# Kernel optimization log

Hardware: AMD Instinct MI355X
Metric: run time of the kernel (lower is better)

The kernel has to match this reference:

```python
import jax, jax.numpy as jnp
import numpy as np
import math

D_MODEL, D_K, D_V = 1024, 64, 64
B, S = 4, 4096


def setup_inputs() -> dict:
    key = jax.random.key(0)
    ks = jax.random.split(key, 7)
    lim = 1.0 / math.sqrt(D_MODEL)
    return {
        "embeddings": jax.random.normal(ks[0], (B, S, D_MODEL), dtype=jnp.float32),
        "Wq": jax.random.uniform(ks[1], (D_MODEL, D_K), minval=-lim, maxval=lim, dtype=jnp.float32),
        "bq": jax.random.uniform(ks[2], (D_K,), minval=-lim, maxval=lim, dtype=jnp.float32),
        "Wk": jax.random.uniform(ks[3], (D_MODEL, D_K), minval=-lim, maxval=lim, dtype=jnp.float32),
        "bk": jax.random.uniform(ks[4], (D_K,), minval=-lim, maxval=lim, dtype=jnp.float32),
        "Wv": jax.random.uniform(ks[5], (D_MODEL, D_V), minval=-lim, maxval=lim, dtype=jnp.float32),
        "bv": jax.random.uniform(ks[6], (D_V,), minval=-lim, maxval=lim, dtype=jnp.float32),
    }


def reference(embeddings, Wq, bq, Wk, bk, Wv, bv):
    # Q, K: [B, S, d_k]; V: [B, S, d_v]
    Q = embeddings @ Wq + bq
    K = embeddings @ Wk + bk
    V = embeddings @ Wv + bv
    scale = 1.0 / math.sqrt(D_K)
    # scores: [B, S, S]
    scores = jnp.einsum("bsk,btk->bst", Q, K) * scale
    attn = jax.nn.softmax(scores, axis=-1)
    return jnp.einsum("bst,btv->bsv", attn, V)
```

## Files before the change

### kernel.cpp

```cpp
#include <hip/hip_runtime.h>

#define SEQ  4096
#define DMODEL 1024
#define QTOT 16384
#define QSCALE 0.18033688011112042f

typedef __bf16 bf16x8 __attribute__((ext_vector_type(8)));
typedef unsigned short u16x8 __attribute__((ext_vector_type(8)));
typedef float f32x4 __attribute__((ext_vector_type(4)));

static __device__ __forceinline__ unsigned short f2bfbits(float f) {
    unsigned int u = __builtin_bit_cast(unsigned int, f);
    unsigned int lsb = (u >> 16) & 1u;
    u += 0x7fffu + lsb;
    return (unsigned short)(u >> 16);
}

static __device__ __forceinline__ bf16x8 ld_frag(const unsigned short* p) {
    uint4 u = *reinterpret_cast<const uint4*>(p);
    return __builtin_bit_cast(bf16x8, u);
}

__global__ void prep_weights(const float* __restrict__ Wq,
                             const float* __restrict__ Wk,
                             const float* __restrict__ Wv,
                             unsigned short* __restrict__ WtS) {
    int o = blockIdx.x * 256 + threadIdx.x;
    int f = o >> 9, q = o & 511;
    int lane = q >> 3, j = q & 7;
    int kc = f / 12, nt = f - kc * 12;
    int n = nt * 16 + (lane & 15);
    int k = kc * 32 + (lane >> 4) * 8 + j;
    float v;
    if (n < 64)       v = Wq[k * 64 + n];
    else if (n < 128) v = Wk[k * 64 + (n - 64)];
    else              v = Wv[k * 64 + (n - 128)];
    WtS[o] = f2bfbits(v);
}

__global__ __launch_bounds__(256) void proj_cs(
        const float* __restrict__ emb, const unsigned short* __restrict__ WtS,
        const float* __restrict__ bq, const float* __restrict__ bk,
        const float* __restrict__ bv,
        unsigned short* __restrict__ Qb, unsigned short* __restrict__ Kb,
        unsigned short* __restrict__ VT) {
    __shared__ __align__(16) unsigned short Et[2][32 * 256];

    const int tid = threadIdx.x;
    const int w = tid >> 6, lane = tid & 63;
    const int c = lane & 15, qd = lane >> 4;
    const int m = w & 1, nh = w >> 1;
    const int mbase = blockIdx.x * 32;

    f32x4 acc[6];
#pragma unroll
    for (int i = 0; i < 6; i++) acc[i] = (f32x4){0.f, 0.f, 0.f, 0.f};

    const unsigned short* wpB = WtS + nh * 3072 + lane * 8;

    {
        float4 g[8];
#pragma unroll
        for (int rr = 0; rr < 8; rr++)
            g[rr] = *reinterpret_cast<const float4*>(
                emb + (size_t)(mbase + w * 8 + rr) * DMODEL + lane * 4);
#pragma unroll
        for (int rr = 0; rr < 8; rr++) {
            int row = w * 8 + rr;
            ushort4 p;
            p.x = f2bfbits(g[rr].x); p.y = f2bfbits(g[rr].y);
            p.z = f2bfbits(g[rr].z); p.w = f2bfbits(g[rr].w);
            int off = (lane * 8) ^ ((row & 7) << 4);
            *reinterpret_cast<ushort4*>(
                reinterpret_cast<char*>(&Et[0][0]) + row * 512 + off) = p;
        }
    }

    bf16x8 wc[6];
#pragma unroll
    for (int jj = 0; jj < 6; jj++) wc[jj] = ld_frag(wpB + jj * 512);

    __syncthreads();

    int cur = 0;
    for (int mega = 0; mega < 4; mega++) {
        float4 g[8];
        if (mega < 3) {
#pragma unroll
            for (int rr = 0; rr < 8; rr++)
                g[rr] = *reinterpret_cast<const float4*>(
                    emb + (size_t)(mbase + w * 8 + rr) * DMODEL
                        + (mega + 1) * 256 + lane * 4);
        }

        const char* Eb = reinterpret_cast<const char*>(&Et[cur][0]);
        bf16x8 aq[8];
#pragma unroll
        for (int ks = 0; ks < 8; ks++) {
            int off = (ks * 64 + qd * 16) ^ ((c & 7) << 4);
            aq[ks] = ld_frag(reinterpret_cast<const unsigned short*>(
                Eb + (m * 16 + c) * 512 + off));
        }

#pragma unroll
        for (int ks = 0; ks < 8; ks++) {
            int s = mega * 8 + ks;
            bf16x8 wn[6];
            if (s < 31) {
#pragma unroll
                for (int jj = 0; jj < 6; jj++)
                    wn[jj] = ld_frag(wpB + (s + 1) * 6144 + jj * 512);
            } else {
#pragma unroll
                for (int jj = 0; jj < 6; jj++) wn[jj] = wc[jj];
            }
#pragma unroll
            for (int jj = 0; jj < 6; jj++)
                acc[jj] = __builtin_amdgcn_mfma_f32_16x16x32_bf16(aq[ks], wc[jj], acc[jj], 0, 0, 0);
#pragma unroll
            for (int jj = 0; jj < 6; jj++) wc[jj] = wn[jj];
        }

        if (mega < 3) {
#pragma unroll
            for (int rr = 0; rr < 8; rr++) {
                int row = w * 8 + rr;
                ushort4 p;
                p.x = f2bfbits(g[rr].x); p.y = f2bfbits(g[rr].y);
                p.z = f2bfbits(g[rr].z); p.w = f2bfbits(g[rr].w);
                int off = (lane * 8) ^ ((row & 7) << 4);
                *reinterpret_cast<ushort4*>(
                    reinterpret_cast<char*>(&Et[cur ^ 1][0]) + row * 512 + off) = p;
            }
        }
        __syncthreads();
        cur ^= 1;
    }

#pragma unroll
    for (int jj = 0; jj < 6; jj++) {
        int n = (nh * 6 + jj) * 16 + c;
        float bias = (n < 64) ? bq[n] : (n < 128) ? bk[n - 64] : bv[n - 128];
        float fac = (n < 64) ? QSCALE : 1.0f;
#pragma unroll
        for (int r = 0; r < 4; r++) {
            int token = mbase + m * 16 + qd * 4 + r;
            unsigned short bits = f2bfbits((acc[jj][r] + bias) * fac);
            if (n < 64)        Qb[(size_t)token * 64 + n] = bits;
            else if (n < 128)  Kb[(size_t)token * 64 + (n - 64)] = bits;
            else {
                int bb = token >> 12, ss = token & 4095;
                VT[((size_t)bb * 64 + (n - 128)) * SEQ + ss] = bits;
            }
        }
    }
}

__global__ __launch_bounds__(512, 2) void attn(
        const unsigned short* __restrict__ Qb, const unsigned short* __restrict__ Kb,
        const unsigned short* __restrict__ VT, float* __restrict__ out) {
    __shared__ __align__(16) unsigned short Pl[8][64 * 72];
    __shared__ float l_all[8][64];

    const int tid = threadIdx.x;
    const int w = tid >> 6, lane = tid & 63;
    const int c = lane & 15, qd = lane >> 4;
    const int g3 = blockIdx.x & 7;
    const int b = g3 >> 1;
    const int qblk = ((blockIdx.x >> 3) << 1) | (g3 & 1);
    const int qbase = qblk * 64;
    const int tstart = w * 512;

    bf16x8 aq0[4], aq1[4];
#pragma unroll
    for (int qs = 0; qs < 4; qs++) {
        const unsigned short* Qp = Qb + ((size_t)(b << 12) + qbase + qs * 16 + c) * 64 + qd * 8;
        aq0[qs] = ld_frag(Qp);
        aq1[qs] = ld_frag(Qp + 32);
    }

    f32x4 acc[16];
#pragma unroll
    for (int i = 0; i < 16; i++) acc[i] = (f32x4){0.f, 0.f, 0.f, 0.f};
    float lsum[4][4];
#pragma unroll
    for (int qs = 0; qs < 4; qs++)
#pragma unroll
        for (int r = 0; r < 4; r++) lsum[qs][r] = 0.f;

    unsigned short* myP = &Pl[w][0];

#pragma unroll 2
    for (int it = 0; it < 8; it++) {
        const int t0 = tstart + it * 64;
        const unsigned short* Kt = Kb + ((size_t)(b << 12) + t0) * 64;

        bf16x8 bk0[4], bk1[4];
#pragma unroll
        for (int ts = 0; ts < 4; ts++) {
            bk0[ts] = ld_frag(Kt + (ts * 16 + c) * 64 + qd * 8);
            bk1[ts] = ld_frag(Kt + (ts * 16 + c) * 64 + 32 + qd * 8);
        }

#pragma unroll
        for (int qs = 0; qs < 4; qs++) {
            f32x4 sc[4];
#pragma unroll
            for (int ts = 0; ts < 4; ts++) {
                f32x4 z = (f32x4){0.f, 0.f, 0.f, 0.f};
                z = __builtin_amdgcn_mfma_f32_16x16x32_bf16(aq0[qs], bk0[ts], z, 0, 0, 0);
                z = __builtin_amdgcn_mfma_f32_16x16x32_bf16(aq1[qs], bk1[ts], z, 0, 0, 0);
                sc[ts] = z;
            }
#pragma unroll
            for (int ts = 0; ts < 4; ts++)
#pragma unroll
                for (int r = 0; r < 4; r++) {
                    float p = __builtin_amdgcn_exp2f(sc[ts][r]);
                    lsum[qs][r] += p;
                    myP[(qs * 16 + qd * 4 + r) * 72 + ts * 16 + c] = f2bfbits(p);
                }
        }

        bf16x8 bv0[4], bv1[4];
#pragma unroll
        for (int nt = 0; nt < 4; nt++) {
            const unsigned short* Vp = VT + (((size_t)b * 64 + nt * 16 + c) << 12) + t0 + qd * 8;
            bv0[nt] = ld_frag(Vp);
            bv1[nt] = ld_frag(Vp + 32);
        }

#pragma unroll
        for (int qs = 0; qs < 4; qs++) {
            bf16x8 ap0 = ld_frag(&myP[(qs * 16 + c) * 72 + qd * 8]);
            bf16x8 ap1 = ld_frag(&myP[(qs * 16 + c) * 72 + 32 + qd * 8]);
#pragma unroll
            for (int nt = 0; nt < 4; nt++) {
                acc[qs * 4 + nt] = __builtin_amdgcn_mfma_f32_16x16x32_bf16(ap0, bv0[nt], acc[qs * 4 + nt], 0, 0, 0);
                acc[qs * 4 + nt] = __builtin_amdgcn_mfma_f32_16x16x32_bf16(ap1, bv1[nt], acc[qs * 4 + nt], 0, 0, 0);
            }
        }
    }

#pragma unroll
    for (int off = 1; off < 16; off <<= 1)
#pragma unroll
        for (int qs = 0; qs < 4; qs++)
#pragma unroll
            for (int r = 0; r < 4; r++) lsum[qs][r] += __shfl_xor(lsum[qs][r], off);
    if (c == 0) {
#pragma unroll
        for (int qs = 0; qs < 4; qs++)
#pragma unroll
            for (int r = 0; r < 4; r++)
                l_all[w][qs * 16 + qd * 4 + r] = lsum[qs][r];
    }

    float* red = (float*)&Pl[0][0];
    __syncthreads();
    if (w >= 4) {
        float* rp = red + (w - 4) * 4352 + lane * 68;
#pragma unroll
        for (int i = 0; i < 16; i++) *reinterpret_cast<f32x4*>(rp + i * 4) = acc[i];
    }
    __syncthreads();
    if (w < 4) {
        float* rp = red + w * 4352 + lane * 68;
#pragma unroll
        for (int i = 0; i < 16; i++) acc[i] += *reinterpret_cast<const f32x4*>(rp + i * 4);
    }
    __syncthreads();
    if (w == 2 || w == 3) {
        float* rp = red + (w - 2) * 4352 + lane * 68;
#pragma unroll
        for (int i = 0; i < 16; i++) *reinterpret_cast<f32x4*>(rp + i * 4) = acc[i];
    }
    __syncthreads();
    if (w < 2) {
        float* rp = red + w * 4352 + lane * 68;
#pragma unroll
        for (int i = 0; i < 16; i++) acc[i] += *reinterpret_cast<const f32x4*>(rp + i * 4);
    }
    __syncthreads();
    if (w == 1) {
        float* rp = red + lane * 68;
#pragma unroll
        for (int i = 0; i < 16; i++) *reinterpret_cast<f32x4*>(rp + i * 4) = acc[i];
    }
    __syncthreads();
    if (w == 0) {
        float* rp = red + lane * 68;
#pragma unroll
        for (int i = 0; i < 16; i++) acc[i] += *reinterpret_cast<const f32x4*>(rp + i * 4);
#pragma unroll
        for (int qs = 0; qs < 4; qs++)
#pragma unroll
            for (int r = 0; r < 4; r++) {
                int q = qs * 16 + qd * 4 + r;
                float l = 0.f;
#pragma unroll
                for (int ww = 0; ww < 8; ww++) l += l_all[ww][q];
                float inv = 1.0f / l;
                size_t row = (size_t)(b << 12) + qbase + q;
#pragma unroll
                for (int nt = 0; nt < 4; nt++)
                    out[row * 64 + nt * 16 + c] = acc[qs * 4 + nt][r] * inv;
            }
    }
}

extern "C" void kernel_launch(void* const* d_in, const int* in_sizes, int n_in,
                              void* d_out, int out_size, void* d_ws, size_t ws_size,
                              hipStream_t stream) {
    const float* emb = (const float*)d_in[0];
    const float* Wq  = (const float*)d_in[1];
    const float* bq  = (const float*)d_in[2];
    const float* Wk  = (const float*)d_in[3];
    const float* bk  = (const float*)d_in[4];
    const float* Wv  = (const float*)d_in[5];
    const float* bv  = (const float*)d_in[6];
    float* out = (float*)d_out;

    unsigned short* ws = (unsigned short*)d_ws;
    unsigned short* WtS = ws;
    unsigned short* Qb = ws + 192 * 1024;
    unsigned short* Kb = Qb + QTOT * 64;
    unsigned short* VT = Kb + QTOT * 64;

    prep_weights<<<768, 256, 0, stream>>>(Wq, Wk, Wv, WtS);
    proj_cs<<<512, 256, 0, stream>>>(emb, WtS, bq, bk, bv, Qb, Kb, VT);
    attn<<<256, 512, 0, stream>>>(Qb, Kb, VT, out);
}
```

Baseline: 153.7 us.

## Split attention key range across two blocks and add finalize reduction kernel

The attention kernel now processes half the key range per block: grid doubles to 512 blocks, each wave covers 256 keys instead of 512. Unnormalized accumulators and row sums are written to workspace, and a new finalize kernel sums the two halves and normalizes. This is meant to raise occupancy across CUs (256 blocks underfilled the device), at the cost of extra global traffic for partials and one more kernel launch. It relies on softmax with no max subtraction, so the partials combine additively.

```diff
diff --git a/kernel.cpp b/kernel.cpp
--- a/kernel.cpp
+++ b/kernel.cpp
@@ -158,7 +158,8 @@
 
 __global__ __launch_bounds__(512, 2) void attn(
         const unsigned short* __restrict__ Qb, const unsigned short* __restrict__ Kb,
-        const unsigned short* __restrict__ VT, float* __restrict__ out) {
+        const unsigned short* __restrict__ VT,
+        float* __restrict__ accP, float* __restrict__ lsumP) {
     __shared__ __align__(16) unsigned short Pl[8][64 * 72];
     __shared__ float l_all[8][64];
 
@@ -167,9 +168,10 @@
     const int c = lane & 15, qd = lane >> 4;
     const int g3 = blockIdx.x & 7;
     const int b = g3 >> 1;
-    const int qblk = ((blockIdx.x >> 3) << 1) | (g3 & 1);
+    const int th = g3 & 1;
+    const int qblk = blockIdx.x >> 3;
     const int qbase = qblk * 64;
-    const int tstart = w * 512;
+    const int tstart = th * 2048 + w * 256;
 
     bf16x8 aq0[4], aq1[4];
 #pragma unroll
@@ -191,7 +193,7 @@
     unsigned short* myP = &Pl[w][0];
 
 #pragma unroll 2
-    for (int it = 0; it < 8; it++) {
+    for (int it = 0; it < 4; it++) {
         const int t0 = tstart + it * 64;
         const unsigned short* Kt = Kb + ((size_t)(b << 12) + t0) * 64;
 
@@ -292,6 +294,8 @@
         float* rp = red + lane * 68;
 #pragma unroll
         for (int i = 0; i < 16; i++) acc[i] += *reinterpret_cast<const f32x4*>(rp + i * 4);
+        float* accOut = accP + (size_t)th * ((size_t)QTOT * 64);
+        float* lOut   = lsumP + (size_t)th * QTOT;
 #pragma unroll
         for (int qs = 0; qs < 4; qs++)
 #pragma unroll
@@ -300,13 +304,29 @@
                 float l = 0.f;
 #pragma unroll
                 for (int ww = 0; ww < 8; ww++) l += l_all[ww][q];
-                float inv = 1.0f / l;
                 size_t row = (size_t)(b << 12) + qbase + q;
+                lOut[row] = l;
 #pragma unroll
                 for (int nt = 0; nt < 4; nt++)
-                    out[row * 64 + nt * 16 + c] = acc[qs * 4 + nt][r] * inv;
-            }
-    }
+                    accOut[row * 64 + nt * 16 + c] = acc[qs * 4 + nt][r];
+            }
+    }
+}
+
+__global__ __launch_bounds__(256) void finalize(
+        const float* __restrict__ accP, const float* __restrict__ lsumP,
+        float* __restrict__ out) {
+    int idx = blockIdx.x * 256 + threadIdx.x;
+    int row = idx >> 4;
+    float4 a0 = reinterpret_cast<const float4*>(accP)[idx];
+    float4 a1 = reinterpret_cast<const float4*>(accP)[idx + QTOT * 16];
+    float inv = 1.0f / (lsumP[row] + lsumP[row + QTOT]);
+    float4 o;
+    o.x = (a0.x + a1.x) * inv;
+    o.y = (a0.y + a1.y) * inv;
+    o.z = (a0.z + a1.z) * inv;
+    o.w = (a0.w + a1.w) * inv;
+    reinterpret_cast<float4*>(out)[idx] = o;
 }
 
 extern "C" void kernel_launch(void* const* d_in, const int* in_sizes, int n_in,
@@ -326,8 +346,11 @@
     unsigned short* Qb = ws + 192 * 1024;
     unsigned short* Kb = Qb + QTOT * 64;
     unsigned short* VT = Kb + QTOT * 64;
+    float* accP  = (float*)(VT + QTOT * 64);
+    float* lsumP = accP + (size_t)2 * QTOT * 64;
 
     prep_weights<<<768, 256, 0, stream>>>(Wq, Wk, Wv, WtS);
     proj_cs<<<512, 256, 0, stream>>>(emb, WtS, bq, bk, bv, Qb, Kb, VT);
-    attn<<<256, 512, 0, stream>>>(Qb, Kb, VT, out);
-}
+    attn<<<512, 512, 0, stream>>>(Qb, Kb, VT, accP, lsumP);
+    finalize<<<1024, 256, 0, stream>>>(accP, lsumP, out);
+}
```

New measurement: 162.5 us. 5.7% more time.

## Double-buffer K fragments, prefetch V early, and raise MFMA wave priority

Applied to the files above, without the earlier changes.

Restructures the attention inner loop into a manually two-stage pipeline. The next tile's K fragments are loaded into alternate registers during the current tile's softmax. V loads are issued at the start of each step instead of after the score computation, and s_setprio is raised around the MFMA blocks. The aim is to hide global-load latency behind compute, at the cost of extra VGPR pressure that could lower occupancy or cause spills.

```diff
diff --git a/kernel.cpp b/kernel.cpp
--- a/kernel.cpp
+++ b/kernel.cpp
@@ -189,58 +189,75 @@
         for (int r = 0; r < 4; r++) lsum[qs][r] = 0.f;
 
     unsigned short* myP = &Pl[w][0];
-
-#pragma unroll 2
-    for (int it = 0; it < 8; it++) {
-        const int t0 = tstart + it * 64;
-        const unsigned short* Kt = Kb + ((size_t)(b << 12) + t0) * 64;
-
-        bf16x8 bk0[4], bk1[4];
-#pragma unroll
-        for (int ts = 0; ts < 4; ts++) {
-            bk0[ts] = ld_frag(Kt + (ts * 16 + c) * 64 + qd * 8);
-            bk1[ts] = ld_frag(Kt + (ts * 16 + c) * 64 + 32 + qd * 8);
-        }
-
-#pragma unroll
-        for (int qs = 0; qs < 4; qs++) {
-            f32x4 sc[4];
-#pragma unroll
-            for (int ts = 0; ts < 4; ts++) {
-                f32x4 z = (f32x4){0.f, 0.f, 0.f, 0.f};
-                z = __builtin_amdgcn_mfma_f32_16x16x32_bf16(aq0[qs], bk0[ts], z, 0, 0, 0);
-                z = __builtin_amdgcn_mfma_f32_16x16x32_bf16(aq1[qs], bk1[ts], z, 0, 0, 0);
-                sc[ts] = z;
-            }
-#pragma unroll
-            for (int ts = 0; ts < 4; ts++)
-#pragma unroll
-                for (int r = 0; r < 4; r++) {
-                    float p = __builtin_amdgcn_exp2f(sc[ts][r]);
-                    lsum[qs][r] += p;
-                    myP[(qs * 16 + qd * 4 + r) * 72 + ts * 16 + c] = f2bfbits(p);
-                }
-        }
-
-        bf16x8 bv0[4], bv1[4];
-#pragma unroll
-        for (int nt = 0; nt < 4; nt++) {
-            const unsigned short* Vp = VT + (((size_t)b * 64 + nt * 16 + c) << 12) + t0 + qd * 8;
-            bv0[nt] = ld_frag(Vp);
-            bv1[nt] = ld_frag(Vp + 32);
-        }
-
-#pragma unroll
-        for (int qs = 0; qs < 4; qs++) {
-            bf16x8 ap0 = ld_frag(&myP[(qs * 16 + c) * 72 + qd * 8]);
-            bf16x8 ap1 = ld_frag(&myP[(qs * 16 + c) * 72 + 32 + qd * 8]);
-#pragma unroll
-            for (int nt = 0; nt < 4; nt++) {
-                acc[qs * 4 + nt] = __builtin_amdgcn_mfma_f32_16x16x32_bf16(ap0, bv0[nt], acc[qs * 4 + nt], 0, 0, 0);
-                acc[qs * 4 + nt] = __builtin_amdgcn_mfma_f32_16x16x32_bf16(ap1, bv1[nt], acc[qs * 4 + nt], 0, 0, 0);
-            }
-        }
-    }
+    const unsigned short* KbB = Kb + (size_t)(b << 12) * 64;
+
+#define LOADK(K0, K1, T0) do {                                               \
+        const unsigned short* Kt_ = KbB + (size_t)(T0) * 64;                 \
+        _Pragma("unroll")                                                    \
+        for (int ts = 0; ts < 4; ts++) {                                     \
+            K0[ts] = ld_frag(Kt_ + (ts * 16 + c) * 64 + qd * 8);             \
+            K1[ts] = ld_frag(Kt_ + (ts * 16 + c) * 64 + 32 + qd * 8);        \
+        } } while (0)
+
+#define ATTN_STEP(T0, CK0, CK1, PF, NK0, NK1, NT0) do {                      \
+        const int t0_ = (T0);                                                \
+                   \
+        bf16x8 bv0_[4], bv1_[4];                                             \
+        _Pragma("unroll")                                                    \
+        for (int nt = 0; nt < 4; nt++) {                                     \
+            const unsigned short* Vp_ =                                      \
+                VT + (((size_t)b * 64 + nt * 16 + c) << 12) + t0_ + qd * 8;  \
+            bv0_[nt] = ld_frag(Vp_);                                         \
+            bv1_[nt] = ld_frag(Vp_ + 32);                                    \
+        }                                                                    \
+             \
+        _Pragma("unroll")                                                    \
+        for (int qs = 0; qs < 4; qs++) {                                     \
+            f32x4 sc_[4];                                                    \
+            __builtin_amdgcn_s_setprio(1);                                   \
+            _Pragma("unroll")                                                \
+            for (int ts = 0; ts < 4; ts++) {                                 \
+                f32x4 z_ = (f32x4){0.f, 0.f, 0.f, 0.f};                      \
+                z_ = __builtin_amdgcn_mfma_f32_16x16x32_bf16(aq0[qs], CK0[ts], z_, 0, 0, 0); \
+                z_ = __builtin_amdgcn_mfma_f32_16x16x32_bf16(aq1[qs], CK1[ts], z_, 0, 0, 0); \
+                sc_[ts] = z_;                                                \
+            }                                                                \
+            __builtin_amdgcn_s_setprio(0);                                   \
+              \
+            if (qs == 0 && (PF)) { LOADK(NK0, NK1, NT0); }                   \
+            _Pragma("unroll")                                                \
+            for (int ts = 0; ts < 4; ts++)                                   \
+                _Pragma("unroll")                                            \
+                for (int r = 0; r < 4; r++) {                                \
+                    float p_ = __builtin_amdgcn_exp2f(sc_[ts][r]);           \
+                    lsum[qs][r] += p_;                                       \
+                    myP[(qs * 16 + qd * 4 + r) * 72 + ts * 16 + c] = f2bfbits(p_); \
+                }                                                            \
+        }                                                                    \
+                           \
+        _Pragma("unroll")                                                    \
+        for (int qs = 0; qs < 4; qs++) {                                     \
+            bf16x8 ap0_ = ld_frag(&myP[(qs * 16 + c) * 72 + qd * 8]);        \
+            bf16x8 ap1_ = ld_frag(&myP[(qs * 16 + c) * 72 + 32 + qd * 8]);   \
+            __builtin_amdgcn_s_setprio(1);                                   \
+            _Pragma("unroll")                                                \
+            for (int nt = 0; nt < 4; nt++) {                                 \
+                acc[qs * 4 + nt] = __builtin_amdgcn_mfma_f32_16x16x32_bf16(ap0_, bv0_[nt], acc[qs * 4 + nt], 0, 0, 0); \
+                acc[qs * 4 + nt] = __builtin_amdgcn_mfma_f32_16x16x32_bf16(ap1_, bv1_[nt], acc[qs * 4 + nt], 0, 0, 0); \
+            }                                                                \
+            __builtin_amdgcn_s_setprio(0);                                   \
+        }                                                                    \
+    } while (0)
+
+    bf16x8 ka0[4], ka1[4], kb0[4], kb1[4];
+    LOADK(ka0, ka1, tstart);
+    for (int ip = 0; ip < 4; ip++) {
+        const int t0 = tstart + ip * 128;
+        ATTN_STEP(t0,      ka0, ka1, 1,        kb0, kb1, t0 + 64);
+        ATTN_STEP(t0 + 64, kb0, kb1, (ip < 3), ka0, ka1, t0 + 128);
+    }
+#undef ATTN_STEP
+#undef LOADK
 
 #pragma unroll
     for (int off = 1; off < 16; off <<= 1)
```

After: 198.3 us. +29.0%, slower.
